# Kernel tuning notes

Measured on AMD Instinct MI355X. Metric: run time of the kernel, lower is better.

The kernel has to match this reference:

```python
import jax, jax.numpy as jnp
import numpy as np

DIM = 2048
N_EXPERTS = 64
TOP_K = 8
BIAS_UPDATE_RATE = 0.01
EPS = 1e-8


def setup_inputs() -> dict:
    key = jax.random.key(0)
    k_x, k_w = jax.random.split(key)
    x = jax.random.normal(k_x, (4, 8192, DIM), dtype=jnp.float32)
    gate_weight = jax.random.normal(k_w, (N_EXPERTS, DIM), dtype=jnp.float32) * 0.02
    adaptive_bias = jnp.zeros((N_EXPERTS,), dtype=jnp.float32)
    expert_usage = jnp.zeros((N_EXPERTS,), dtype=jnp.float32)
    return {"x": x, "gate_weight": gate_weight, "adaptive_bias": adaptive_bias,
            "expert_usage": expert_usage}


def reference(x, gate_weight, adaptive_bias, expert_usage):
    B, S, D = x.shape
    xf = x.reshape(-1, D)                                   # [T, D]
    scores = jnp.einsum('td,ed->te', xf, gate_weight)       # [T, E]
    scores = scores + adaptive_bias[None, :]
    probs = jax.nn.softmax(scores, axis=-1)
    top_w, top_idx = jax.lax.top_k(probs, TOP_K)            # [T, K]
    top_w = top_w / (jnp.sum(top_w, axis=-1, keepdims=True) + EPS)
    # training-mode adaptive-bias update (no-grad histogram of selected experts)
    usage = jnp.bincount(top_idx.reshape(-1), length=N_EXPERTS).astype(jnp.float32)
    usage = usage / (B * S * TOP_K)
    usage_diff = usage - 1.0 / N_EXPERTS
    new_adaptive_bias = adaptive_bias - BIAS_UPDATE_RATE * usage_diff
    new_expert_usage = 0.9 * expert_usage + 0.1 * usage
    top_w = top_w.reshape(B, S, TOP_K)
    top_idx = top_idx.reshape(B, S, TOP_K)
    return top_w, top_idx, new_adaptive_bias, new_expert_usage
```

## Files before the change

kernel.cpp:

```cpp
#include <hip/hip_runtime.h>
#include <math.h>

constexpr int DIM    = 2048;
constexpr int NEXP   = 64;
constexpr int TOPK   = 8;
constexpr int T_TOT  = 32768;

constexpr int TTILE  = 64;
constexpr int BK     = 32;
constexpr int XST    = 66;
constexpr int SST    = 68;

constexpr size_t OFF_W   = 0;
constexpr size_t OFF_IDX = (size_t)T_TOT * TOPK;
constexpr size_t OFF_B   = OFF_IDX * 2;
constexpr size_t OFF_U   = OFF_B + NEXP;

__global__ __launch_bounds__(256, 2)
void moe_gate_main(const float* __restrict__ x,
                   const float* __restrict__ gw,
                   const float* __restrict__ bias,
                   float* __restrict__ out,
                   unsigned int* __restrict__ cnt)
{
    __shared__ double smem[2 * BK * XST];
    __shared__ unsigned int hist[NEXP];

    const int tid = threadIdx.x;
    const int t0  = blockIdx.x * TTILE;
    const int eg  = tid & 15;
    const int tg  = tid >> 4;

    if (tid < NEXP) hist[tid] = 0;

    double acc[4][4];
    #pragma unroll
    for (int i = 0; i < 4; ++i)
        #pragma unroll
        for (int j = 0; j < 4; ++j) acc[i][j] = 0.0;

    double* Wd = smem;
    double* Xd = smem + BK * XST;

    for (int k0 = 0; k0 < DIM; k0 += BK) {
        __syncthreads();
        #pragma unroll
        for (int s = 0; s < 2; ++s) {
            const int f = tid + s * 256;
            const int r = f >> 3;
            const int c = (f & 7) << 2;
            const float4 wv = *reinterpret_cast<const float4*>(gw + (size_t)r * DIM + k0 + c);
            const float4 xv = *reinterpret_cast<const float4*>(x + (size_t)(t0 + r) * DIM + k0 + c);
            Wd[(c + 0) * XST + r] = (double)wv.x;
            Wd[(c + 1) * XST + r] = (double)wv.y;
            Wd[(c + 2) * XST + r] = (double)wv.z;
            Wd[(c + 3) * XST + r] = (double)wv.w;
            Xd[(c + 0) * XST + r] = (double)xv.x;
            Xd[(c + 1) * XST + r] = (double)xv.y;
            Xd[(c + 2) * XST + r] = (double)xv.z;
            Xd[(c + 3) * XST + r] = (double)xv.w;
        }
        __syncthreads();

        #pragma unroll 4
        for (int k = 0; k < BK; ++k) {
            const double* wp = Wd + k * XST + 4 * eg;
            const double* xp = Xd + k * XST + 4 * tg;
            const double w0 = wp[0], w1 = wp[1], w2 = wp[2], w3 = wp[3];
            const double x0 = xp[0], x1 = xp[1], x2 = xp[2], x3 = xp[3];
            acc[0][0] = fma(w0, x0, acc[0][0]);
            acc[0][1] = fma(w0, x1, acc[0][1]);
            acc[0][2] = fma(w0, x2, acc[0][2]);
            acc[0][3] = fma(w0, x3, acc[0][3]);
            acc[1][0] = fma(w1, x0, acc[1][0]);
            acc[1][1] = fma(w1, x1, acc[1][1]);
            acc[1][2] = fma(w1, x2, acc[1][2]);
            acc[1][3] = fma(w1, x3, acc[1][3]);
            acc[2][0] = fma(w2, x0, acc[2][0]);
            acc[2][1] = fma(w2, x1, acc[2][1]);
            acc[2][2] = fma(w2, x2, acc[2][2]);
            acc[2][3] = fma(w2, x3, acc[2][3]);
            acc[3][0] = fma(w3, x0, acc[3][0]);
            acc[3][1] = fma(w3, x1, acc[3][1]);
            acc[3][2] = fma(w3, x2, acc[3][2]);
            acc[3][3] = fma(w3, x3, acc[3][3]);
        }
    }

    __syncthreads();
    float* S = reinterpret_cast<float*>(smem);
    #pragma unroll
    for (int ei = 0; ei < 4; ++ei) {
        const int e = 4 * eg + ei;
        const float b = bias[e];
        float4 v;
        v.x = (float)acc[ei][0] + b;
        v.y = (float)acc[ei][1] + b;
        v.z = (float)acc[ei][2] + b;
        v.w = (float)acc[ei][3] + b;
        *reinterpret_cast<float4*>(S + e * SST + 4 * tg) = v;
    }
    __syncthreads();

    if (tid < TTILE) {
        const int t = tid;
        float bv[TOPK];
        int   bi[TOPK];
        #pragma unroll
        for (int j = 0; j < TOPK; ++j) { bv[j] = -INFINITY; bi[j] = 0; }

        for (int e = 0; e < NEXP; ++e) {
            const float v = S[e * SST + t];
            if (v > bv[TOPK - 1]) {
                bv[TOPK - 1] = v; bi[TOPK - 1] = e;
                #pragma unroll
                for (int j = TOPK - 1; j > 0; --j) {
                    if (bv[j] > bv[j - 1]) {
                        const float tv = bv[j]; bv[j] = bv[j - 1]; bv[j - 1] = tv;
                        const int   ti = bi[j]; bi[j] = bi[j - 1]; bi[j - 1] = ti;
                    }
                }
            }
        }

        const float m = bv[0];
        float Z = 0.0f;
        for (int e = 0; e < NEXP; ++e) Z += expf(S[e * SST + t] - m);
        const float rZ = 1.0f / Z;

        float p[TOPK];
        float ws = 0.0f;
        #pragma unroll
        for (int j = 0; j < TOPK; ++j) { p[j] = expf(bv[j] - m) * rZ; ws += p[j]; }
        const float rd = 1.0f / (ws + 1e-8f);

        const size_t tglob = (size_t)(t0 + t);
        float4 w0 = { p[0] * rd, p[1] * rd, p[2] * rd, p[3] * rd };
        float4 w1 = { p[4] * rd, p[5] * rd, p[6] * rd, p[7] * rd };
        *reinterpret_cast<float4*>(out + OFF_W + tglob * TOPK)     = w0;
        *reinterpret_cast<float4*>(out + OFF_W + tglob * TOPK + 4) = w1;
        float4 i0 = { (float)bi[0], (float)bi[1], (float)bi[2], (float)bi[3] };
        float4 i1 = { (float)bi[4], (float)bi[5], (float)bi[6], (float)bi[7] };
        *reinterpret_cast<float4*>(out + OFF_IDX + tglob * TOPK)     = i0;
        *reinterpret_cast<float4*>(out + OFF_IDX + tglob * TOPK + 4) = i1;

        #pragma unroll
        for (int j = 0; j < TOPK; ++j) atomicAdd(&hist[bi[j]], 1u);
    }

    __syncthreads();
    if (tid < NEXP) atomicAdd(cnt + tid, hist[tid]);
}

__global__ void moe_gate_fin(const unsigned int* __restrict__ cnt,
                             const float* __restrict__ bias,
                             const float* __restrict__ eu,
                             float* __restrict__ out)
{
    const int e = threadIdx.x;
    const float usage = (float)cnt[e] * (1.0f / (float)(T_TOT * TOPK));
    out[OFF_B + e] = bias[e] - 0.01f * (usage - 1.0f / (float)NEXP);
    out[OFF_U + e] = 0.9f * eu[e] + 0.1f * usage;
}

extern "C" void kernel_launch(void* const* d_in, const int* in_sizes, int n_in,
                              void* d_out, int out_size, void* d_ws, size_t ws_size,
                              hipStream_t stream) {
    const float* x    = (const float*)d_in[0];
    const float* gw   = (const float*)d_in[1];
    const float* bias = (const float*)d_in[2];
    const float* eu   = (const float*)d_in[3];
    float* out = (float*)d_out;
    unsigned int* cnt = (unsigned int*)d_ws;

    hipMemsetAsync(cnt, 0, NEXP * sizeof(unsigned int), stream);
    moe_gate_main<<<T_TOT / TTILE, 256, 0, stream>>>(x, gw, bias, out, cnt);
    moe_gate_fin<<<1, NEXP, 0, stream>>>(cnt, bias, eu, out);
}
```

Baseline: 576.9 us.

## Switch gating GEMM to FP32 with async LDS loads and FP64 refinement of near-ties

```diff
diff --git a/kernel.cpp b/kernel.cpp
--- a/kernel.cpp
+++ b/kernel.cpp
@@ -7,149 +7,266 @@
 constexpr int T_TOT  = 32768;
 
 constexpr int TTILE  = 64;
-constexpr int BK     = 32;
-constexpr int XST    = 66;
-constexpr int SST    = 68;
+constexpr int BK     = 64;
+constexpr int NSTEP  = DIM / BK;
+
+constexpr float GAP_TH = 5.0e-4f;
 
 constexpr size_t OFF_W   = 0;
 constexpr size_t OFF_IDX = (size_t)T_TOT * TOPK;
 constexpr size_t OFF_B   = OFF_IDX * 2;
 constexpr size_t OFF_U   = OFF_B + NEXP;
+
+
+__device__ __forceinline__ void gl2lds16(const void* g, void* l) {
+    __builtin_amdgcn_global_load_lds(
+        (const __attribute__((address_space(1))) void*)g,
+        (__attribute__((address_space(3))) void*)l, 16, 0, 0);
+}
+
+#define MAC(i, j, A, B) \
+    acc[i][j] = fmaf(A.x, B.x, acc[i][j]); \
+    acc[i][j] = fmaf(A.y, B.y, acc[i][j]); \
+    acc[i][j] = fmaf(A.z, B.z, acc[i][j]); \
+    acc[i][j] = fmaf(A.w, B.w, acc[i][j]);
 
 __global__ __launch_bounds__(256, 2)
 void moe_gate_main(const float* __restrict__ x,
                    const float* __restrict__ gw,
                    const float* __restrict__ bias,
                    float* __restrict__ out,
-                   unsigned int* __restrict__ cnt)
+                   unsigned int* __restrict__ ws)
 {
-    __shared__ double smem[2 * BK * XST];
+    __shared__ __align__(16) char smem[65536];
     __shared__ unsigned int hist[NEXP];
 
     const int tid = threadIdx.x;
     const int t0  = blockIdx.x * TTILE;
-    const int eg  = tid & 15;
-    const int tg  = tid >> 4;
 
     if (tid < NEXP) hist[tid] = 0;
 
-    double acc[4][4];
+    const int l   = tid & 63;
+    const int wv  = tid >> 6;
+    const int c16 = l & 15;
+    const int rs  = l >> 4;
+
+    const char* xrow[4];
+    const char* wrow[4];
+    int ldsoff[4];
+    #pragma unroll
+    for (int s = 0; s < 4; ++s) {
+        const int r  = 16 * s + 4 * wv + rs;
+        const int cc = ((c16 ^ (r & 7)) << 4);
+        ldsoff[s] = r * 256 + c16 * 16;
+        xrow[s] = (const char*)x  + (size_t)(t0 + r) * (DIM * 4) + cc;
+        wrow[s] = (const char*)gw + (size_t)r        * (DIM * 4) + cc;
+    }
+
+    char* const W0 = smem;
+    char* const X0 = smem + 16384;
+    char* const W1 = smem + 32768;
+    char* const X1 = smem + 49152;
+
+    float acc[4][4];
     #pragma unroll
     for (int i = 0; i < 4; ++i)
         #pragma unroll
-        for (int j = 0; j < 4; ++j) acc[i][j] = 0.0;
-
-    double* Wd = smem;
-    double* Xd = smem + BK * XST;
-
-    for (int k0 = 0; k0 < DIM; k0 += BK) {
-        __syncthreads();
-        #pragma unroll
-        for (int s = 0; s < 2; ++s) {
-            const int f = tid + s * 256;
-            const int r = f >> 3;
-            const int c = (f & 7) << 2;
-            const float4 wv = *reinterpret_cast<const float4*>(gw + (size_t)r * DIM + k0 + c);
-            const float4 xv = *reinterpret_cast<const float4*>(x + (size_t)(t0 + r) * DIM + k0 + c);
-            Wd[(c + 0) * XST + r] = (double)wv.x;
-            Wd[(c + 1) * XST + r] = (double)wv.y;
-            Wd[(c + 2) * XST + r] = (double)wv.z;
-            Wd[(c + 3) * XST + r] = (double)wv.w;
-            Xd[(c + 0) * XST + r] = (double)xv.x;
-            Xd[(c + 1) * XST + r] = (double)xv.y;
-            Xd[(c + 2) * XST + r] = (double)xv.z;
-            Xd[(c + 3) * XST + r] = (double)xv.w;
-        }
-        __syncthreads();
-
-        #pragma unroll 4
-        for (int k = 0; k < BK; ++k) {
-            const double* wp = Wd + k * XST + 4 * eg;
-            const double* xp = Xd + k * XST + 4 * tg;
-            const double w0 = wp[0], w1 = wp[1], w2 = wp[2], w3 = wp[3];
-            const double x0 = xp[0], x1 = xp[1], x2 = xp[2], x3 = xp[3];
-            acc[0][0] = fma(w0, x0, acc[0][0]);
-            acc[0][1] = fma(w0, x1, acc[0][1]);
-            acc[0][2] = fma(w0, x2, acc[0][2]);
-            acc[0][3] = fma(w0, x3, acc[0][3]);
-            acc[1][0] = fma(w1, x0, acc[1][0]);
-            acc[1][1] = fma(w1, x1, acc[1][1]);
-            acc[1][2] = fma(w1, x2, acc[1][2]);
-            acc[1][3] = fma(w1, x3, acc[1][3]);
-            acc[2][0] = fma(w2, x0, acc[2][0]);
-            acc[2][1] = fma(w2, x1, acc[2][1]);
-            acc[2][2] = fma(w2, x2, acc[2][2]);
-            acc[2][3] = fma(w2, x3, acc[2][3]);
-            acc[3][0] = fma(w3, x0, acc[3][0]);
-            acc[3][1] = fma(w3, x1, acc[3][1]);
-            acc[3][2] = fma(w3, x2, acc[3][2]);
-            acc[3][3] = fma(w3, x3, acc[3][3]);
+        for (int j = 0; j < 4; ++j) acc[i][j] = 0.0f;
+
+    #pragma unroll
+    for (int s = 0; s < 4; ++s) {
+        gl2lds16(xrow[s], X0 + ldsoff[s]);
+        gl2lds16(wrow[s], W0 + ldsoff[s]);
+    }
+
+    const int eg = tid & 15;
+    const int tg = tid >> 4;
+    const int wx = (eg & 7) << 4;
+    const int tx = (tg & 7) << 4;
+
+    #pragma unroll 2
+    for (int step = 0; step < NSTEP; ++step) {
+        __syncthreads();
+        const int cur = step & 1;
+        const char* Wl = cur ? W1 : W0;
+        const char* Xl = cur ? X1 : X0;
+        if (step + 1 < NSTEP) {
+            char* Wn = cur ? W0 : W1;
+            char* Xn = cur ? X0 : X1;
+            const size_t kadd = (size_t)(step + 1) * (BK * 4);
+            #pragma unroll
+            for (int s = 0; s < 4; ++s) {
+                gl2lds16(xrow[s] + kadd, Xn + ldsoff[s]);
+                gl2lds16(wrow[s] + kadd, Wn + ldsoff[s]);
+            }
+        }
+        const char* wb = Wl + eg * 256;
+        const char* xb = Xl + tg * 256;
+        #pragma unroll
+        for (int q = 0; q < 16; ++q) {
+            const int wq = (q << 4) ^ wx;
+            const int xq = (q << 4) ^ tx;
+            const float4 a0 = *(const float4*)(wb + wq);
+            const float4 a1 = *(const float4*)(wb + 4096  + wq);
+            const float4 a2 = *(const float4*)(wb + 8192  + wq);
+            const float4 a3 = *(const float4*)(wb + 12288 + wq);
+            const float4 b0 = *(const float4*)(xb + xq);
+            const float4 b1 = *(const float4*)(xb + 4096  + xq);
+            const float4 b2 = *(const float4*)(xb + 8192  + xq);
+            const float4 b3 = *(const float4*)(xb + 12288 + xq);
+            MAC(0,0,a0,b0) MAC(0,1,a0,b1) MAC(0,2,a0,b2) MAC(0,3,a0,b3)
+            MAC(1,0,a1,b0) MAC(1,1,a1,b1) MAC(1,2,a1,b2) MAC(1,3,a1,b3)
+            MAC(2,0,a2,b0) MAC(2,1,a2,b1) MAC(2,2,a2,b2) MAC(2,3,a2,b3)
+            MAC(3,0,a3,b0) MAC(3,1,a3,b1) MAC(3,2,a3,b2) MAC(3,3,a3,b3)
         }
     }
 
     __syncthreads();
-    float* S = reinterpret_cast<float*>(smem);
-    #pragma unroll
-    for (int ei = 0; ei < 4; ++ei) {
-        const int e = 4 * eg + ei;
+    float* S = (float*)smem;
+    #pragma unroll
+    for (int i = 0; i < 4; ++i) {
+        const int e = eg + 16 * i;
         const float b = bias[e];
-        float4 v;
-        v.x = (float)acc[ei][0] + b;
-        v.y = (float)acc[ei][1] + b;
-        v.z = (float)acc[ei][2] + b;
-        v.w = (float)acc[ei][3] + b;
-        *reinterpret_cast<float4*>(S + e * SST + 4 * tg) = v;
+        #pragma unroll
+        for (int j = 0; j < 4; ++j)
+            S[e * 65 + tg + 16 * j] = acc[i][j] + b;
     }
     __syncthreads();
 
     if (tid < TTILE) {
         const int t = tid;
-        float bv[TOPK];
-        int   bi[TOPK];
-        #pragma unroll
-        for (int j = 0; j < TOPK; ++j) { bv[j] = -INFINITY; bi[j] = 0; }
-
+        float bv[9]; int bi[9];
+        #pragma unroll
+        for (int j = 0; j < 9; ++j) { bv[j] = -INFINITY; bi[j] = 0; }
         for (int e = 0; e < NEXP; ++e) {
-            const float v = S[e * SST + t];
-            if (v > bv[TOPK - 1]) {
-                bv[TOPK - 1] = v; bi[TOPK - 1] = e;
+            const float v = S[e * 65 + t];
+            if (v > bv[8]) {
+                bv[8] = v; bi[8] = e;
                 #pragma unroll
-                for (int j = TOPK - 1; j > 0; --j) {
+                for (int j = 8; j > 0; --j) {
                     if (bv[j] > bv[j - 1]) {
-                        const float tv = bv[j]; bv[j] = bv[j - 1]; bv[j - 1] = tv;
-                        const int   ti = bi[j]; bi[j] = bi[j - 1]; bi[j - 1] = ti;
+                        const float tv = bv[j]; bv[j] = bv[j-1]; bv[j-1] = tv;
+                        const int   ti = bi[j]; bi[j] = bi[j-1]; bi[j-1] = ti;
                     }
                 }
             }
         }
+        float ming = bv[0] - bv[1];
+        #pragma unroll
+        for (int j = 1; j < 8; ++j) ming = fminf(ming, bv[j] - bv[j + 1]);
+        const bool amb = (ming < GAP_TH);
 
         const float m = bv[0];
         float Z = 0.0f;
-        for (int e = 0; e < NEXP; ++e) Z += expf(S[e * SST + t] - m);
+        for (int e = 0; e < NEXP; ++e) Z += expf(S[e * 65 + t] - m);
         const float rZ = 1.0f / Z;
-
-        float p[TOPK];
-        float ws = 0.0f;
-        #pragma unroll
-        for (int j = 0; j < TOPK; ++j) { p[j] = expf(bv[j] - m) * rZ; ws += p[j]; }
-        const float rd = 1.0f / (ws + 1e-8f);
+        float p[TOPK]; float wsum = 0.0f;
+        #pragma unroll
+        for (int j = 0; j < TOPK; ++j) { p[j] = expf(bv[j] - m) * rZ; wsum += p[j]; }
+        const float rd = 1.0f / (wsum + 1e-8f);
 
         const size_t tglob = (size_t)(t0 + t);
-        float4 w0 = { p[0] * rd, p[1] * rd, p[2] * rd, p[3] * rd };
-        float4 w1 = { p[4] * rd, p[5] * rd, p[6] * rd, p[7] * rd };
-        *reinterpret_cast<float4*>(out + OFF_W + tglob * TOPK)     = w0;
-        *reinterpret_cast<float4*>(out + OFF_W + tglob * TOPK + 4) = w1;
+        float4 w0 = { p[0]*rd, p[1]*rd, p[2]*rd, p[3]*rd };
+        float4 w1 = { p[4]*rd, p[5]*rd, p[6]*rd, p[7]*rd };
+        *(float4*)(out + OFF_W + tglob * TOPK)     = w0;
+        *(float4*)(out + OFF_W + tglob * TOPK + 4) = w1;
         float4 i0 = { (float)bi[0], (float)bi[1], (float)bi[2], (float)bi[3] };
         float4 i1 = { (float)bi[4], (float)bi[5], (float)bi[6], (float)bi[7] };
-        *reinterpret_cast<float4*>(out + OFF_IDX + tglob * TOPK)     = i0;
-        *reinterpret_cast<float4*>(out + OFF_IDX + tglob * TOPK + 4) = i1;
-
-        #pragma unroll
-        for (int j = 0; j < TOPK; ++j) atomicAdd(&hist[bi[j]], 1u);
+        *(float4*)(out + OFF_IDX + tglob * TOPK)     = i0;
+        *(float4*)(out + OFF_IDX + tglob * TOPK + 4) = i1;
+
+        if (!amb) {
+            #pragma unroll
+            for (int j = 0; j < TOPK; ++j) atomicAdd(&hist[bi[j]], 1u);
+        } else {
+            const unsigned slot = atomicAdd(ws + NEXP, 1u);
+            ws[NEXP + 1 + slot] = (unsigned)tglob;
+        }
     }
 
     __syncthreads();
-    if (tid < NEXP) atomicAdd(cnt + tid, hist[tid]);
+    if (tid < NEXP) atomicAdd(ws + tid, hist[tid]);
+}
+
+__global__ __launch_bounds__(256)
+void moe_gate_refine(const float* __restrict__ x,
+                     const float* __restrict__ gw,
+                     const float* __restrict__ bias,
+                     float* __restrict__ out,
+                     unsigned int* __restrict__ ws)
+{
+    __shared__ __align__(16) float xs[DIM];
+    __shared__ float S[NEXP];
+    const unsigned nflag = ws[NEXP];
+    const unsigned* list = ws + NEXP + 1;
+
+    for (unsigned ii = blockIdx.x; ii < nflag; ii += gridDim.x) {
+        const size_t t = (size_t)list[ii];
+        __syncthreads();
+        #pragma unroll
+        for (int jj = 0; jj < 2; ++jj) {
+            const int f = threadIdx.x + jj * 256;
+            ((float4*)xs)[f] = ((const float4*)(x + t * DIM))[f];
+        }
+        __syncthreads();
+
+        const int e = threadIdx.x >> 2;
+        const int q = threadIdx.x & 3;
+        const float* wr = gw + (size_t)e * DIM + q * 512;
+        const float* xr = xs + q * 512;
+        double s = 0.0;
+        for (int k = 0; k < 512; k += 4) {
+            const float4 wv4 = *(const float4*)(wr + k);
+            const float4 xv4 = *(const float4*)(xr + k);
+            s = fma((double)wv4.x, (double)xv4.x, s);
+            s = fma((double)wv4.y, (double)xv4.y, s);
+            s = fma((double)wv4.z, (double)xv4.z, s);
+            s = fma((double)wv4.w, (double)xv4.w, s);
+        }
+        s += __shfl_down(s, 2, 4);
+        s += __shfl_down(s, 1, 4);
+        if (q == 0) S[e] = (float)s + bias[e];
+        __syncthreads();
+
+        if (threadIdx.x == 0) {
+            float bv[TOPK]; int bi[TOPK];
+            #pragma unroll
+            for (int j = 0; j < TOPK; ++j) { bv[j] = -INFINITY; bi[j] = 0; }
+            for (int e2 = 0; e2 < NEXP; ++e2) {
+                const float v = S[e2];
+                if (v > bv[TOPK - 1]) {
+                    bv[TOPK - 1] = v; bi[TOPK - 1] = e2;
+                    #pragma unroll
+                    for (int j = TOPK - 1; j > 0; --j) {
+                        if (bv[j] > bv[j - 1]) {
+                            const float tv = bv[j]; bv[j] = bv[j-1]; bv[j-1] = tv;
+                            const int   ti = bi[j]; bi[j] = bi[j-1]; bi[j-1] = ti;
+                        }
+                    }
+                }
+            }
+            const float m = bv[0];
+            float Z = 0.0f;
+            for (int e2 = 0; e2 < NEXP; ++e2) Z += expf(S[e2] - m);
+            const float rZ = 1.0f / Z;
+            float p[TOPK]; float wsum = 0.0f;
+            #pragma unroll
+            for (int j = 0; j < TOPK; ++j) { p[j] = expf(bv[j] - m) * rZ; wsum += p[j]; }
+            const float rd = 1.0f / (wsum + 1e-8f);
+
+            float4 w0 = { p[0]*rd, p[1]*rd, p[2]*rd, p[3]*rd };
+            float4 w1 = { p[4]*rd, p[5]*rd, p[6]*rd, p[7]*rd };
+            *(float4*)(out + OFF_W + t * TOPK)     = w0;
+            *(float4*)(out + OFF_W + t * TOPK + 4) = w1;
+            float4 i0 = { (float)bi[0], (float)bi[1], (float)bi[2], (float)bi[3] };
+            float4 i1 = { (float)bi[4], (float)bi[5], (float)bi[6], (float)bi[7] };
+            *(float4*)(out + OFF_IDX + t * TOPK)     = i0;
+            *(float4*)(out + OFF_IDX + t * TOPK + 4) = i1;
+
+            #pragma unroll
+            for (int j = 0; j < TOPK; ++j) atomicAdd(ws + bi[j], 1u);
+        }
+    }
 }
 
 __global__ void moe_gate_fin(const unsigned int* __restrict__ cnt,
@@ -173,7 +290,8 @@
     float* out = (float*)d_out;
     unsigned int* cnt = (unsigned int*)d_ws;
 
-    hipMemsetAsync(cnt, 0, NEXP * sizeof(unsigned int), stream);
+    hipMemsetAsync(cnt, 0, (NEXP + 1) * sizeof(unsigned int), stream);
     moe_gate_main<<<T_TOT / TTILE, 256, 0, stream>>>(x, gw, bias, out, cnt);
+    moe_gate_refine<<<256, 256, 0, stream>>>(x, gw, bias, out, cnt);
     moe_gate_fin<<<1, NEXP, 0, stream>>>(cnt, bias, eu, out);
 }
```

After: 1.585 ms. +174.7%, slower.
